# Kernel optimization log

Measured on AMD Instinct MI355X. Metric: run time of the kernel, lower is better.

The kernel has to match this reference:

```python
import jax, jax.numpy as jnp
import numpy as np

B, N, C, H, W = 4, 262144, 40, 256, 256
HID = 128


def _bilinear_sample(plane, u, v):
    """torch F.grid_sample(mode='bilinear', padding_mode='zeros', align_corners=False).
    plane: (B, C, H, W); u, v: (B, N) in [-1, 1] (u -> width axis, v -> height axis).
    Returns (B, N, C)."""
    Wd, Hd = plane.shape[3], plane.shape[2]
    ix = ((u + 1.0) * Wd - 1.0) * 0.5
    iy = ((v + 1.0) * Hd - 1.0) * 0.5
    ix0 = jnp.floor(ix)
    iy0 = jnp.floor(iy)
    fx = ix - ix0
    fy = iy - iy0
    ix0 = ix0.astype(jnp.int32)
    iy0 = iy0.astype(jnp.int32)
    flat = plane.reshape(plane.shape[0], plane.shape[1], Hd * Wd)  # (B,C,H*W)

    def corner(xi, yi, w):
        valid = (xi >= 0) & (xi < Wd) & (yi >= 0) & (yi < Hd)
        xc = jnp.clip(xi, 0, Wd - 1)
        yc = jnp.clip(yi, 0, Hd - 1)
        idx = yc * Wd + xc  # (B,N)
        vals = jnp.take_along_axis(flat, idx[:, None, :], axis=2)  # (B,C,N)
        return vals * (w * valid)[:, None, :]

    out = (corner(ix0, iy0, (1 - fx) * (1 - fy))
           + corner(ix0 + 1, iy0, fx * (1 - fy))
           + corner(ix0, iy0 + 1, (1 - fx) * fy)
           + corner(ix0 + 1, iy0 + 1, fx * fy))  # (B,C,N)
    return jnp.transpose(out, (0, 2, 1))  # (B,N,C)


def _sample_triplane(triplane, coords):
    x, y, z = coords[..., 0], coords[..., 1], coords[..., 2]
    f_xy = _bilinear_sample(triplane[:, 0], x, y)
    f_xz = _bilinear_sample(triplane[:, 1], x, z)
    f_yz = _bilinear_sample(triplane[:, 2], y, z)
    return jnp.concatenate([f_xy, f_xz, f_yz], axis=-1)  # (B,N,3C)


def setup_inputs() -> dict:
    key = jax.random.key(0)
    ks = jax.random.split(key, 16)
    triplane = jax.random.normal(ks[0], (B, 3, C, H, W), dtype=jnp.float32)
    coords = jax.random.uniform(ks[1], (B, N, 3), dtype=jnp.float32) * 2.0 - 1.0
    vd = jax.random.normal(ks[2], (B, N, 3), dtype=jnp.float32)
    view_dirs = vd / (jnp.linalg.norm(vd, axis=-1, keepdims=True) + 1e-8)
    s = 0.05
    p = {
        'triplane': triplane, 'coords': coords, 'view_dirs': view_dirs,
        'dw1': jax.random.normal(ks[3], (3 * C, HID), dtype=jnp.float32) * s,
        'db1': jnp.zeros((HID,), jnp.float32),
        'dw2': jax.random.normal(ks[4], (HID, HID), dtype=jnp.float32) * s,
        'db2': jnp.zeros((HID,), jnp.float32),
        'dw3': jax.random.normal(ks[5], (HID, 1), dtype=jnp.float32) * s,
        'db3': jnp.zeros((1,), jnp.float32),
        'cw1': jax.random.normal(ks[6], (3 * C + 3, HID), dtype=jnp.float32) * s,
        'cb1': jnp.zeros((HID,), jnp.float32),
        'cw2': jax.random.normal(ks[7], (HID, HID), dtype=jnp.float32) * s,
        'cb2': jnp.zeros((HID,), jnp.float32),
        'cw3': jax.random.normal(ks[8], (HID, 3), dtype=jnp.float32) * s,
        'cb3': jnp.zeros((3,), jnp.float32),
    }
    return p


def reference(triplane, coords, view_dirs, dw1, db1, dw2, db2, dw3, db3,
              cw1, cb1, cw2, cb2, cw3, cb3):
    feats = _sample_triplane(triplane, coords)  # (B,N,3C)
    h = jax.nn.relu(feats @ dw1 + db1)
    h = jax.nn.relu(h @ dw2 + db2)
    density = h @ dw3 + db3  # (B,N,1)
    cin = jnp.concatenate([feats, view_dirs], axis=-1)
    g = jax.nn.relu(cin @ cw1 + cb1)
    g = jax.nn.relu(g @ cw2 + cb2)
    rgb = jax.nn.sigmoid(g @ cw3 + cb3)  # (B,N,3)
    return density, rgb
```

## Files before the change

### kernel.cpp

```cpp
#include <hip/hip_runtime.h>
#include <cstdint>
#include <cstddef>

typedef __bf16 bf16x8 __attribute__((ext_vector_type(8)));
typedef float  f32x4  __attribute__((ext_vector_type(4)));

#define MFMA16(a,b,c) __builtin_amdgcn_mfma_f32_16x16x32_bf16((a),(b),(c),0,0,0)

__device__ __forceinline__ uint f2bf1(float f){
  uint u = __builtin_bit_cast(uint, f);
  u += 0x7FFFu + ((u >> 16) & 1u);
  return u >> 16;
}
__device__ __forceinline__ uint pack2(float a, float b){
  return f2bf1(a) | (f2bf1(b) << 16);
}
__device__ __forceinline__ uint pack2f(float a, float b){
  uint ua = __builtin_bit_cast(uint, a) + 0x8000u;
  uint ub = __builtin_bit_cast(uint, b) + 0x8000u;
  return __builtin_amdgcn_perm(ub, ua, 0x07060302u);
}
__device__ __forceinline__ float bflo(uint d){ return __builtin_bit_cast(float, d << 16); }
__device__ __forceinline__ float bfhi(uint d){ return __builtin_bit_cast(float, d & 0xFFFF0000u); }

__global__ __launch_bounds__(256, 4) void prep_k(
    const float* __restrict__ tri, ushort* __restrict__ tp,
    const float* __restrict__ dw1, const float* __restrict__ cw1,
    const float* __restrict__ dw2, const float* __restrict__ cw2,
    const float* __restrict__ dw3, const float* __restrict__ cw3,
    uint4* __restrict__ wpk)
{
  __shared__ uint stu[40 * 130];
  const int tid = threadIdx.x;
  if (blockIdx.x < 3072){
    const int y = blockIdx.x & 255;
    const int q = blockIdx.x >> 8;
    const float* src = tri + (size_t)q * 40 * 65536 + y * 256;
#pragma unroll
    for (int it = 0; it < 10; it++){
      int lin = it * 256 + tid;
      int c = lin >> 6, xq = lin & 63;
      const float4 v = *(const float4*)(src + (size_t)c * 65536 + xq * 4);
      uint2 w; w.x = pack2(v.x, v.y); w.y = pack2(v.z, v.w);
      *(uint2*)&stu[c * 130 + 2 * xq] = w;
    }
    __syncthreads();
    uint4* dst = (uint4*)(tp + ((size_t)q * 65536 + (size_t)y * 256) * 40);
#pragma unroll
    for (int it = 0; it < 5; it++){
      int m = it * 256 + tid;
      uint4 o;
#pragma unroll
      for (int jj = 0; jj < 4; jj++){
        int d  = 4 * m + jj;
        int x  = (d * 3277) >> 16;
        int cp = d - x * 20;
        uint A = stu[(2 * cp    ) * 130 + (x >> 1)];
        uint B = stu[(2 * cp + 1) * 130 + (x >> 1)];
        ((uint*)&o)[jj] = (x & 1) ? ((A >> 16)      | (B & 0xFFFF0000u))
                                  : ((A & 0xFFFFu)  | (B << 16));
      }
      dst[m] = o;
    }
  } else {
    int idx = (blockIdx.x - 3072) * 256 + tid;
    if (idx >= 8704) return;
    int mode, rel;
    if      (idx < 2048){ mode = 0; rel = idx; }
    else if (idx < 4096){ mode = 1; rel = idx - 2048; }
    else if (idx < 6144){ mode = 2; rel = idx - 4096; }
    else if (idx < 8192){ mode = 3; rel = idx - 6144; }
    else if (idx < 8448){ mode = 4; rel = idx - 8192; }
    else                { mode = 5; rel = idx - 8448; }
    int frag = rel >> 6, lane = rel & 63;
    int Mt = frag >> 2, s = frag & 3;
    int m  = Mt * 16 + (lane & 15);
    int kb = s * 32 + (lane >> 4) * 8;
    uint d[4];
#pragma unroll
    for (int jj = 0; jj < 4; jj++){
      float v0 = 0.f, v1 = 0.f;
#pragma unroll
      for (int h = 0; h < 2; h++){
        int k = kb + jj * 2 + h;
        float v = 0.f;
        switch (mode){
          case 0: v = (k < 120) ? dw1[k * 128 + m] : 0.f; break;
          case 1: v = (k < 123) ? cw1[k * 128 + m] : 0.f; break;
          case 2: v = dw2[k * 128 + m]; break;
          case 3: v = cw2[k * 128 + m]; break;
          case 4: v = (m == 0) ? dw3[k] : 0.f; break;
          default: v = (m >= 1 && m <= 3) ? cw3[k * 3 + (m - 1)] : 0.f; break;
        }
        if (h == 0) v0 = v; else v1 = v;
      }
      d[jj] = pack2(v0, v1);
    }
    uint4 o; o.x = d[0]; o.y = d[1]; o.z = d[2]; o.w = d[3];
    wpk[idx] = o;
  }
}

__device__ __forceinline__ uint4 blend4(uint4 a, uint4 b, uint4 c, uint4 d,
                                        float w00, float w10, float w01, float w11){
  uint4 ov;
  ov.x = pack2f(w00*bflo(a.x)+w10*bflo(b.x)+w01*bflo(c.x)+w11*bflo(d.x),
                w00*bfhi(a.x)+w10*bfhi(b.x)+w01*bfhi(c.x)+w11*bfhi(d.x));
  ov.y = pack2f(w00*bflo(a.y)+w10*bflo(b.y)+w01*bflo(c.y)+w11*bflo(d.y),
                w00*bfhi(a.y)+w10*bfhi(b.y)+w01*bfhi(c.y)+w11*bfhi(d.y));
  ov.z = pack2f(w00*bflo(a.z)+w10*bflo(b.z)+w01*bflo(c.z)+w11*bflo(d.z),
                w00*bfhi(a.z)+w10*bfhi(b.z)+w01*bfhi(c.z)+w11*bfhi(d.z));
  ov.w = pack2f(w00*bflo(a.w)+w10*bflo(b.w)+w01*bflo(c.w)+w11*bflo(d.w),
                w00*bfhi(a.w)+w10*bfhi(b.w)+w01*bfhi(c.w)+w11*bfhi(d.w));
  return ov;
}

__device__ __forceinline__ bf16x8 read_h(const uint* S, int s, int t, int lrow, int lq){
  int dwb = (s * 16 + lq * 4 + (lrow << 2)) & 63;
  return __builtin_bit_cast(bf16x8, *(const uint4*)&S[(t * 16 + lrow) * 64 + dwb]);
}

__device__ __forceinline__ void put_h(uint* S, f32x4 v, int Mt, int t, int lrow, int lq){
  uint2 w;
  w.x = pack2f(fmaxf(v[0], 0.f), fmaxf(v[1], 0.f));
  w.y = pack2f(fmaxf(v[2], 0.f), fmaxf(v[3], 0.f));
  int dw = (Mt * 8 + lq * 2 + (lrow << 2)) & 63;
  *(uint2*)&S[(t * 16 + lrow) * 64 + dw] = w;
}

__device__ __forceinline__ void stage16(const uint4* __restrict__ g, uint4* l,
                                        int wave, int lane, int nchunk){
  for (int c = wave; c < nchunk; c += 4){
    __builtin_amdgcn_global_load_lds(
      (const __attribute__((address_space(1))) void*)(g + c * 64 + lane),
      (__attribute__((address_space(3))) void*)(l + c * 64 + lane), 16, 0, 0);
  }
}

__device__ __forceinline__ void layer1_half(uint* S, const uint4* W,
                                            const float* __restrict__ bias,
                                            const uint4 (&bf)[4][2], int half,
                                            int lrow, int lq, int lane){
  f32x4 acc[4][2];
#pragma unroll
  for (int mt = 0; mt < 4; mt++){
    f32x4 bi = *(const f32x4*)(bias + (half * 4 + mt) * 16 + lq * 4);
    acc[mt][0] = bi; acc[mt][1] = bi;
  }
#pragma unroll
  for (int s = 0; s < 4; s++)
#pragma unroll
    for (int mt = 0; mt < 4; mt++){
      bf16x8 aw = __builtin_bit_cast(bf16x8, W[(mt * 4 + s) * 64 + lane]);
      acc[mt][0] = MFMA16(aw, __builtin_bit_cast(bf16x8, bf[s][0]), acc[mt][0]);
      acc[mt][1] = MFMA16(aw, __builtin_bit_cast(bf16x8, bf[s][1]), acc[mt][1]);
    }
#pragma unroll
  for (int mt = 0; mt < 4; mt++){
    put_h(S, acc[mt][0], half * 4 + mt, 0, lrow, lq);
    put_h(S, acc[mt][1], half * 4 + mt, 1, lrow, lq);
  }
}

__device__ __forceinline__ void load_hb(const uint* S, bf16x8 (&hb)[4][2],
                                        int lrow, int lq){
#pragma unroll
  for (int s = 0; s < 4; s++){
    hb[s][0] = read_h(S, s, 0, lrow, lq);
    hb[s][1] = read_h(S, s, 1, lrow, lq);
  }
}

__device__ __forceinline__ void dense_half(uint* S, const uint4* W,
                                           const float* __restrict__ bias,
                                           const bf16x8 (&hb)[4][2], int half,
                                           int lrow, int lq, int lane){
  f32x4 acc[4][2];
#pragma unroll
  for (int mt = 0; mt < 4; mt++){
    f32x4 bi = *(const f32x4*)(bias + (half * 4 + mt) * 16 + lq * 4);
    acc[mt][0] = bi; acc[mt][1] = bi;
  }
#pragma unroll
  for (int s = 0; s < 4; s++)
#pragma unroll
    for (int mt = 0; mt < 4; mt++){
      bf16x8 aw = __builtin_bit_cast(bf16x8, W[(mt * 4 + s) * 64 + lane]);
      acc[mt][0] = MFMA16(aw, hb[s][0], acc[mt][0]);
      acc[mt][1] = MFMA16(aw, hb[s][1], acc[mt][1]);
    }
#pragma unroll
  for (int mt = 0; mt < 4; mt++){
    put_h(S, acc[mt][0], half * 4 + mt, 0, lrow, lq);
    put_h(S, acc[mt][1], half * 4 + mt, 1, lrow, lq);
  }
}

__device__ __forceinline__ void out_l(const uint* S, const uint4* W,
                                      f32x4 (&acc3)[2], int lrow, int lq, int lane){
#pragma unroll
  for (int s = 0; s < 4; s++){
    bf16x8 aw = __builtin_bit_cast(bf16x8, W[s * 64 + lane]);
    acc3[0] = MFMA16(aw, read_h(S, s, 0, lrow, lq), acc3[0]);
    acc3[1] = MFMA16(aw, read_h(S, s, 1, lrow, lq), acc3[1]);
  }
}

__global__ __launch_bounds__(256, 2) void fused_k(
    const ushort* __restrict__ tp, const float* __restrict__ coords,
    const float* __restrict__ vdirs, const uint4* __restrict__ wpk,
    const float* __restrict__ db1, const float* __restrict__ db2,
    const float* __restrict__ db3, const float* __restrict__ cb1,
    const float* __restrict__ cb2, const float* __restrict__ cb3,
    float* __restrict__ out)
{
  __shared__ uint  Sh[4][2048];
  __shared__ uint4 WB[2][1024];
  const int wave = threadIdx.x >> 6;
  uint* S = Sh[wave];
  const int lane = threadIdx.x & 63, lrow = lane & 15, lq = lane >> 4;
  const int blk   = blockIdx.x;
  const int pbase = (blk & 3) * 262144 + (blk >> 2) * 128 + wave * 32;

  stage16(wpk + 0, WB[0], wave, lane, 16);

  uint4 bf[4][2];
#pragma unroll
  for (int t = 0; t < 2; t++){
    const int p  = pbase + t * 16 + lrow;
    const int bb = p >> 18;
    const float cx = coords[3 * p], cy = coords[3 * p + 1], cz = coords[3 * p + 2];
    float pw00[3], pw10[3], pw01[3], pw11[3];
    uint  o00[3], o10[3], o01[3], o11[3];
#pragma unroll
    for (int pl = 0; pl < 3; pl++){
      const float u = (pl == 2) ? cy : cx;
      const float v = (pl == 0) ? cy : cz;
      float ix = fmaf(u, 128.f, 127.5f);
      float iy = fmaf(v, 128.f, 127.5f);
      float fx0 = floorf(ix), fy0 = floorf(iy);
      float fx = ix - fx0, fy = iy - fy0;
      int x0 = (int)fx0, y0 = (int)fy0;
      float wx0 = (x0 >= 0  && x0 < 256) ? (1.f - fx) : 0.f;
      float wx1 = (x0 >= -1 && x0 < 255) ? fx : 0.f;
      float wy0 = (y0 >= 0  && y0 < 256) ? (1.f - fy) : 0.f;
      float wy1 = (y0 >= -1 && y0 < 255) ? fy : 0.f;
      int xc0 = min(max(x0, 0), 255), xc1 = min(max(x0 + 1, 0), 255);
      int yc0 = min(max(y0, 0), 255), yc1 = min(max(y0 + 1, 0), 255);
      pw00[pl] = wx0 * wy0; pw10[pl] = wx1 * wy0;
      pw01[pl] = wx0 * wy1; pw11[pl] = wx1 * wy1;
      o00[pl] = ((uint)yc0 * 256u + (uint)xc0) * 40u;
      o10[pl] = ((uint)yc0 * 256u + (uint)xc1) * 40u;
      o01[pl] = ((uint)yc1 * 256u + (uint)xc0) * 40u;
      o11[pl] = ((uint)yc1 * 256u + (uint)xc1) * 40u;
    }
#pragma unroll
    for (int s = 0; s < 4; s++){
      const int chunk = s * 4 + lq;
      if (chunk == 15){
        const float v0 = vdirs[3 * p], v1 = vdirs[3 * p + 1], v2 = vdirs[3 * p + 2];
        uint4 tt; tt.x = pack2f(v0, v1); tt.y = pack2f(v2, 0.f); tt.z = 0u; tt.w = 0u;
        bf[s][t] = tt;
      } else {
        const int pl = (chunk < 5) ? 0 : (chunk < 10) ? 1 : 2;
        const int c0 = chunk * 8 - pl * 40;
        const ushort* base = tp + (size_t)(bb * 3 + pl) * 2621440 + c0;
        uint4 a = *(const uint4*)(base + o00[pl]);
        uint4 b = *(const uint4*)(base + o10[pl]);
        uint4 c = *(const uint4*)(base + o01[pl]);
        uint4 d = *(const uint4*)(base + o11[pl]);
        bf[s][t] = blend4(a, b, c, d, pw00[pl], pw10[pl], pw01[pl], pw11[pl]);
      }
    }
  }

  f32x4 acc3[2];
  {
    float i0 = (lq == 0) ? db3[0] : 0.f;
    float i1 = (lq == 0) ? cb3[0] : 0.f;
    float i2 = (lq == 0) ? cb3[1] : 0.f;
    float i3 = (lq == 0) ? cb3[2] : 0.f;
    f32x4 iv = {i0, i1, i2, i3};
    acc3[0] = iv; acc3[1] = iv;
  }

  __syncthreads();
  stage16(wpk + 1024, WB[1], wave, lane, 16);
  layer1_half(S, WB[0], db1, bf, 0, lrow, lq, lane);
  __syncthreads();
  stage16(wpk + 4096, WB[0], wave, lane, 16);
  layer1_half(S, WB[1], db1, bf, 1, lrow, lq, lane);
  __syncthreads();
  stage16(wpk + 5120, WB[1], wave, lane, 16);
  bf16x8 hb[4][2];
  load_hb(S, hb, lrow, lq);
  dense_half(S, WB[0], db2, hb, 0, lrow, lq, lane);
  __syncthreads();
  stage16(wpk + 8192, WB[0], wave, lane, 4);
  dense_half(S, WB[1], db2, hb, 1, lrow, lq, lane);
  __syncthreads();
  stage16(wpk + 2048, WB[1], wave, lane, 16);
  out_l(S, WB[0], acc3, lrow, lq, lane);
  __syncthreads();
  stage16(wpk + 3072, WB[0], wave, lane, 16);
  layer1_half(S, WB[1], cb1, bf, 0, lrow, lq, lane);
  __syncthreads();
  stage16(wpk + 6144, WB[1], wave, lane, 16);
  layer1_half(S, WB[0], cb1, bf, 1, lrow, lq, lane);
  __syncthreads();
  stage16(wpk + 7168, WB[0], wave, lane, 16);
  bf16x8 hb2[4][2];
  load_hb(S, hb2, lrow, lq);
  dense_half(S, WB[1], cb2, hb2, 0, lrow, lq, lane);
  __syncthreads();
  stage16(wpk + 8448, WB[1], wave, lane, 4);
  dense_half(S, WB[0], cb2, hb2, 1, lrow, lq, lane);
  __syncthreads();
  out_l(S, WB[1], acc3, lrow, lq, lane);

  if (lq == 0){
#pragma unroll
    for (int t = 0; t < 2; t++){
      int p = pbase + t * 16 + lrow;
      out[p] = acc3[t][0];
      float* rgb = out + 1048576 + (size_t)p * 3;
      rgb[0] = 1.f / (1.f + __expf(-acc3[t][1]));
      rgb[1] = 1.f / (1.f + __expf(-acc3[t][2]));
      rgb[2] = 1.f / (1.f + __expf(-acc3[t][3]));
    }
  }
}

extern "C" void kernel_launch(void* const* d_in, const int* in_sizes, int n_in,
                              void* d_out, int out_size, void* d_ws, size_t ws_size,
                              hipStream_t stream)
{
  (void)in_sizes; (void)n_in; (void)out_size; (void)ws_size;
  const float* tri    = (const float*)d_in[0];
  const float* coords = (const float*)d_in[1];
  const float* vdirs  = (const float*)d_in[2];
  const float* dw1 = (const float*)d_in[3];  const float* db1 = (const float*)d_in[4];
  const float* dw2 = (const float*)d_in[5];  const float* db2 = (const float*)d_in[6];
  const float* dw3 = (const float*)d_in[7];  const float* db3 = (const float*)d_in[8];
  const float* cw1 = (const float*)d_in[9];  const float* cb1 = (const float*)d_in[10];
  const float* cw2 = (const float*)d_in[11]; const float* cb2 = (const float*)d_in[12];
  const float* cw3 = (const float*)d_in[13]; const float* cb3 = (const float*)d_in[14];

  char* ws = (char*)d_ws;
  const size_t planes_bytes = 62914560;
  ushort* tp  = (ushort*)ws;
  uint4*  wpk = (uint4*)(ws + planes_bytes);

  prep_k<<<3106, 256, 0, stream>>>(tri, tp, dw1, cw1, dw2, cw2, dw3, cw3, wpk);
  fused_k<<<8192, 256, 0, stream>>>(tp, coords, vdirs, wpk,
                                    db1, db2, db3, cb1, cb2, cb3,
                                    (float*)d_out);
}
```

Baseline: 580.7 us.

## Split weight staging into quarter tiles to halve LDS weight buffer

Splits each 128-wide layer into four quarter tiles instead of two halves, so the double-buffered weight LDS buffer shrinks from 32 KB to 16 KB. The smaller LDS footprint may allow more resident blocks per CU, which would give more latency hiding for the gather-heavy sampling. The cost is twice as many block barriers and smaller staging transfers per step.

```diff
diff --git a/kernel.cpp b/kernel.cpp
--- a/kernel.cpp
+++ b/kernel.cpp
@@ -137,28 +137,28 @@
   }
 }
 
-__device__ __forceinline__ void layer1_half(uint* S, const uint4* W,
-                                            const float* __restrict__ bias,
-                                            const uint4 (&bf)[4][2], int half,
-                                            int lrow, int lq, int lane){
-  f32x4 acc[4][2];
-#pragma unroll
-  for (int mt = 0; mt < 4; mt++){
-    f32x4 bi = *(const f32x4*)(bias + (half * 4 + mt) * 16 + lq * 4);
+__device__ __forceinline__ void layer1_q(uint* S, const uint4* W,
+                                         const float* __restrict__ bias,
+                                         const uint4 (&bf)[4][2], int q,
+                                         int lrow, int lq, int lane){
+  f32x4 acc[2][2];
+#pragma unroll
+  for (int mt = 0; mt < 2; mt++){
+    f32x4 bi = *(const f32x4*)(bias + (q * 2 + mt) * 16 + lq * 4);
     acc[mt][0] = bi; acc[mt][1] = bi;
   }
 #pragma unroll
   for (int s = 0; s < 4; s++)
 #pragma unroll
-    for (int mt = 0; mt < 4; mt++){
+    for (int mt = 0; mt < 2; mt++){
       bf16x8 aw = __builtin_bit_cast(bf16x8, W[(mt * 4 + s) * 64 + lane]);
       acc[mt][0] = MFMA16(aw, __builtin_bit_cast(bf16x8, bf[s][0]), acc[mt][0]);
       acc[mt][1] = MFMA16(aw, __builtin_bit_cast(bf16x8, bf[s][1]), acc[mt][1]);
     }
 #pragma unroll
-  for (int mt = 0; mt < 4; mt++){
-    put_h(S, acc[mt][0], half * 4 + mt, 0, lrow, lq);
-    put_h(S, acc[mt][1], half * 4 + mt, 1, lrow, lq);
+  for (int mt = 0; mt < 2; mt++){
+    put_h(S, acc[mt][0], q * 2 + mt, 0, lrow, lq);
+    put_h(S, acc[mt][1], q * 2 + mt, 1, lrow, lq);
   }
 }
 
@@ -171,28 +171,28 @@
   }
 }
 
-__device__ __forceinline__ void dense_half(uint* S, const uint4* W,
-                                           const float* __restrict__ bias,
-                                           const bf16x8 (&hb)[4][2], int half,
-                                           int lrow, int lq, int lane){
-  f32x4 acc[4][2];
-#pragma unroll
-  for (int mt = 0; mt < 4; mt++){
-    f32x4 bi = *(const f32x4*)(bias + (half * 4 + mt) * 16 + lq * 4);
+__device__ __forceinline__ void dense_q(uint* S, const uint4* W,
+                                        const float* __restrict__ bias,
+                                        const bf16x8 (&hb)[4][2], int q,
+                                        int lrow, int lq, int lane){
+  f32x4 acc[2][2];
+#pragma unroll
+  for (int mt = 0; mt < 2; mt++){
+    f32x4 bi = *(const f32x4*)(bias + (q * 2 + mt) * 16 + lq * 4);
     acc[mt][0] = bi; acc[mt][1] = bi;
   }
 #pragma unroll
   for (int s = 0; s < 4; s++)
 #pragma unroll
-    for (int mt = 0; mt < 4; mt++){
+    for (int mt = 0; mt < 2; mt++){
       bf16x8 aw = __builtin_bit_cast(bf16x8, W[(mt * 4 + s) * 64 + lane]);
       acc[mt][0] = MFMA16(aw, hb[s][0], acc[mt][0]);
       acc[mt][1] = MFMA16(aw, hb[s][1], acc[mt][1]);
     }
 #pragma unroll
-  for (int mt = 0; mt < 4; mt++){
-    put_h(S, acc[mt][0], half * 4 + mt, 0, lrow, lq);
-    put_h(S, acc[mt][1], half * 4 + mt, 1, lrow, lq);
+  for (int mt = 0; mt < 2; mt++){
+    put_h(S, acc[mt][0], q * 2 + mt, 0, lrow, lq);
+    put_h(S, acc[mt][1], q * 2 + mt, 1, lrow, lq);
   }
 }
 
@@ -215,14 +215,14 @@
     float* __restrict__ out)
 {
   __shared__ uint  Sh[4][2048];
-  __shared__ uint4 WB[2][1024];
+  __shared__ uint4 WB[2][512];
   const int wave = threadIdx.x >> 6;
   uint* S = Sh[wave];
   const int lane = threadIdx.x & 63, lrow = lane & 15, lq = lane >> 4;
   const int blk   = blockIdx.x;
   const int pbase = (blk & 3) * 262144 + (blk >> 2) * 128 + wave * 32;
 
-  stage16(wpk + 0, WB[0], wave, lane, 16);
+  stage16(wpk + 0, WB[0], wave, lane, 8);
 
   uint4 bf[4][2];
 #pragma unroll
@@ -285,36 +285,60 @@
   }
 
   __syncthreads();
-  stage16(wpk + 1024, WB[1], wave, lane, 16);
-  layer1_half(S, WB[0], db1, bf, 0, lrow, lq, lane);
-  __syncthreads();
-  stage16(wpk + 4096, WB[0], wave, lane, 16);
-  layer1_half(S, WB[1], db1, bf, 1, lrow, lq, lane);
-  __syncthreads();
-  stage16(wpk + 5120, WB[1], wave, lane, 16);
+  stage16(wpk + 512, WB[1], wave, lane, 8);
+  layer1_q(S, WB[0], db1, bf, 0, lrow, lq, lane);
+  __syncthreads();
+  stage16(wpk + 1024, WB[0], wave, lane, 8);
+  layer1_q(S, WB[1], db1, bf, 1, lrow, lq, lane);
+  __syncthreads();
+  stage16(wpk + 1536, WB[1], wave, lane, 8);
+  layer1_q(S, WB[0], db1, bf, 2, lrow, lq, lane);
+  __syncthreads();
+  stage16(wpk + 4096, WB[0], wave, lane, 8);
+  layer1_q(S, WB[1], db1, bf, 3, lrow, lq, lane);
+  __syncthreads();
+  stage16(wpk + 4608, WB[1], wave, lane, 8);
   bf16x8 hb[4][2];
   load_hb(S, hb, lrow, lq);
-  dense_half(S, WB[0], db2, hb, 0, lrow, lq, lane);
+  dense_q(S, WB[0], db2, hb, 0, lrow, lq, lane);
+  __syncthreads();
+  stage16(wpk + 5120, WB[0], wave, lane, 8);
+  dense_q(S, WB[1], db2, hb, 1, lrow, lq, lane);
+  __syncthreads();
+  stage16(wpk + 5632, WB[1], wave, lane, 8);
+  dense_q(S, WB[0], db2, hb, 2, lrow, lq, lane);
   __syncthreads();
   stage16(wpk + 8192, WB[0], wave, lane, 4);
-  dense_half(S, WB[1], db2, hb, 1, lrow, lq, lane);
-  __syncthreads();
-  stage16(wpk + 2048, WB[1], wave, lane, 16);
+  dense_q(S, WB[1], db2, hb, 3, lrow, lq, lane);
+  __syncthreads();
+  stage16(wpk + 2048, WB[1], wave, lane, 8);
   out_l(S, WB[0], acc3, lrow, lq, lane);
   __syncthreads();
-  stage16(wpk + 3072, WB[0], wave, lane, 16);
-  layer1_half(S, WB[1], cb1, bf, 0, lrow, lq, lane);
-  __syncthreads();
-  stage16(wpk + 6144, WB[1], wave, lane, 16);
-  layer1_half(S, WB[0], cb1, bf, 1, lrow, lq, lane);
-  __syncthreads();
-  stage16(wpk + 7168, WB[0], wave, lane, 16);
+  stage16(wpk + 2560, WB[0], wave, lane, 8);
+  layer1_q(S, WB[1], cb1, bf, 0, lrow, lq, lane);
+  __syncthreads();
+  stage16(wpk + 3072, WB[1], wave, lane, 8);
+  layer1_q(S, WB[0], cb1, bf, 1, lrow, lq, lane);
+  __syncthreads();
+  stage16(wpk + 3584, WB[0], wave, lane, 8);
+  layer1_q(S, WB[1], cb1, bf, 2, lrow, lq, lane);
+  __syncthreads();
+  stage16(wpk + 6144, WB[1], wave, lane, 8);
+  layer1_q(S, WB[0], cb1, bf, 3, lrow, lq, lane);
+  __syncthreads();
+  stage16(wpk + 6656, WB[0], wave, lane, 8);
   bf16x8 hb2[4][2];
   load_hb(S, hb2, lrow, lq);
-  dense_half(S, WB[1], cb2, hb2, 0, lrow, lq, lane);
+  dense_q(S, WB[1], cb2, hb2, 0, lrow, lq, lane);
+  __syncthreads();
+  stage16(wpk + 7168, WB[1], wave, lane, 8);
+  dense_q(S, WB[0], cb2, hb2, 1, lrow, lq, lane);
+  __syncthreads();
+  stage16(wpk + 7680, WB[0], wave, lane, 8);
+  dense_q(S, WB[1], cb2, hb2, 2, lrow, lq, lane);
   __syncthreads();
   stage16(wpk + 8448, WB[1], wave, lane, 4);
-  dense_half(S, WB[0], cb2, hb2, 1, lrow, lq, lane);
+  dense_q(S, WB[0], cb2, hb2, 3, lrow, lq, lane);
   __syncthreads();
   out_l(S, WB[1], acc3, lrow, lq, lane);
 
```

New measurement: 607.8 us. +4.7%, slower.
